# Performance work log

Hardware: AMD Instinct MI355X
Metric: run time of the kernel (lower is better)

The kernel has to match this reference:

```python
import jax, jax.numpy as jnp
import numpy as np

SEQ_LEN = 2048
EMB = 512
BATCH = 8


def _xavier_uniform(key, shape):
    fan_in, fan_out = shape[0], shape[1]
    bound = float(np.sqrt(6.0 / (fan_in + fan_out)))
    return jax.random.uniform(key, shape, dtype=jnp.float32, minval=-bound, maxval=bound)


def setup_inputs() -> dict:
    key = jax.random.key(0)
    kx, k1, k2 = jax.random.split(key, 3)
    x = jax.random.normal(kx, (BATCH, EMB, SEQ_LEN), dtype=jnp.float32)
    weight1 = _xavier_uniform(k1, (EMB, EMB))
    weight2 = _xavier_uniform(k2, (EMB, EMB))
    return {"x": x, "weight1": weight1, "weight2": weight2}


def reference(x, weight1, weight2):
    # x: [b, e, s]
    s = x.shape[-1]
    # projections: O(b*s*e^2)
    fitnesses1 = jnp.einsum('bes,ef->bfs', x, weight1)   # [b, e, s]
    fitnesses2 = jnp.einsum('bfs,ef->bes', x, weight2)   # [b, e, s]
    # s x t interaction matrix: O(b*s^2*e)
    weight = jnp.einsum('bes,bet->bst', fitnesses1, fitnesses2)  # [b, s, t]
    # zero strictly-upper triangle (t > s), as in torch.triu(..., diagonal=1)
    mask = jnp.triu(jnp.ones((s, s), dtype=bool), k=1)
    weight = jnp.where(mask, jnp.zeros((), dtype=weight.dtype), weight)
    fitnesses = jnp.einsum('bst,bet->bes', weight, x)    # [b, e, s]
    avg_fitness = jnp.einsum('bes,bes->be', x, fitnesses)[..., None]  # [b, e, 1]
    net_fitnesses = fitnesses - avg_fitness
    x_next = x + x * net_fitnesses
    return jax.nn.relu(x_next)
```

## Files before the change

### kernel.cpp

```cpp
#include <hip/hip_runtime.h>
#include <hip/hip_bf16.h>
#include <stdint.h>


#define SEQ 2048
#define EMB 512
#define NBATCH 8

typedef unsigned short u16;
typedef __bf16 bf16x8 __attribute__((ext_vector_type(8)));
typedef float f32x4 __attribute__((ext_vector_type(4)));
typedef u16 u16x8 __attribute__((ext_vector_type(8)));

#define AS1 __attribute__((address_space(1)))
#define AS3 __attribute__((address_space(3)))

#define SBAR do { __builtin_amdgcn_sched_barrier(0); __builtin_amdgcn_s_barrier(); \
                  __builtin_amdgcn_sched_barrier(0); } while (0)
#define LGKM0 do { asm volatile("s_waitcnt lgkmcnt(0)" ::: "memory"); \
                   __builtin_amdgcn_sched_barrier(0); } while (0)

__device__ __forceinline__ u16 f2bf(float f) {
  uint32_t u = __builtin_bit_cast(uint32_t, f);
  uint32_t r = u + 0x7FFFu + ((u >> 16) & 1u);
  return (u16)(r >> 16);
}
__device__ __forceinline__ float bf2f(u16 u) {
  return __builtin_bit_cast(float, (uint32_t)u << 16);
}
__device__ __forceinline__ void gld_lds16(const void* g, void* l) {
  __builtin_amdgcn_global_load_lds((AS1 uint32_t*)g, (AS3 uint32_t*)l, 16, 0, 0);
}

__global__ __launch_bounds__(256) void prep_x_kernel(const float* __restrict__ x,
    u16* __restrict__ xb, u16* __restrict__ xbT) {
  __shared__ float tile[64][65];
  const int b = blockIdx.z;
  const int s0 = blockIdx.x * 64, e0 = blockIdx.y * 64;
  const float* xin = x + (size_t)b * EMB * SEQ;
  const int tid = threadIdx.x;
  #pragma unroll
  for (int it = 0; it < 4; ++it) {
    int idx = it * 256 + tid;
    int r = idx >> 4, c4 = idx & 15;
    float4 v = *(const float4*)(xin + (size_t)(e0 + r) * SEQ + s0 + c4 * 4);
    tile[r][c4 * 4 + 0] = v.x; tile[r][c4 * 4 + 1] = v.y;
    tile[r][c4 * 4 + 2] = v.z; tile[r][c4 * 4 + 3] = v.w;
  }
  __syncthreads();
  u16* ob = xb + (size_t)b * EMB * SEQ;
  #pragma unroll
  for (int it = 0; it < 2; ++it) {
    int idx = it * 256 + tid; int r = idx >> 3, c8 = idx & 7;
    u16x8 o;
    #pragma unroll
    for (int q = 0; q < 8; ++q) o[q] = f2bf(tile[r][c8 * 8 + q]);
    *(u16x8*)(ob + (size_t)(e0 + r) * SEQ + s0 + c8 * 8) = o;
  }
  u16* obT = xbT + (size_t)b * SEQ * EMB;
  #pragma unroll
  for (int it = 0; it < 2; ++it) {
    int idx = it * 256 + tid; int r = idx >> 3, c8 = idx & 7;
    u16x8 o;
    #pragma unroll
    for (int q = 0; q < 8; ++q) o[q] = f2bf(tile[c8 * 8 + q][r]);
    *(u16x8*)(obT + (size_t)(s0 + r) * EMB + e0 + c8 * 8) = o;
  }
}

__global__ __launch_bounds__(256) void prep_w_kernel(const float* __restrict__ W1,
    const float* __restrict__ W2, u16* __restrict__ Wcat) {
  __shared__ float tile[32][33];
  const int c0 = blockIdx.x * 32, r0 = blockIdx.y * 32;
  const int tx = threadIdx.x, ty = threadIdx.y;
  if (blockIdx.z == 0) {
    #pragma unroll
    for (int i = 0; i < 32; i += 8)
      tile[ty + i][tx] = W1[(size_t)(r0 + ty + i) * EMB + c0 + tx];
    __syncthreads();
    #pragma unroll
    for (int i = 0; i < 32; i += 8)
      Wcat[(size_t)(c0 + ty + i) * EMB + r0 + tx] = f2bf(tile[tx][ty + i]);
  } else {
    u16* W2b = Wcat + (size_t)512 * 512;
    #pragma unroll
    for (int i = 0; i < 32; i += 8)
      W2b[(size_t)(r0 + ty + i) * EMB + c0 + tx] =
          f2bf(W2[(size_t)(r0 + ty + i) * EMB + c0 + tx]);
  }
}

struct Smem {
  __align__(16) u16 LA[2][256 * 64];
  __align__(16) u16 LB[2][256 * 64];
};

template<typename PAR>
__device__ __forceinline__ void gemm_pipe(PAR par, int nk, Smem& sm, f32x4 (&acc)[8][4]) {
  const int tid  = threadIdx.x;
  const int lane = tid & 63;
  const int wave = tid >> 6;
  const int wr = wave >> 2;
  const int wc = wave & 3;

  auto stage_half = [&](int t, int ab, int half, u16* lds) {
    const u16* g; int ld, k;
    par(t, ab, g, ld, k);
    #pragma unroll
    for (int p = 0; p < 2; ++p) {
      int c = p * 512 + tid;
      int row = c >> 3, cc = c & 7;
      int cs = cc ^ (row & 7);
      gld_lds16(g + (size_t)(half * 128 + row) * ld + k + cs * 8,
                lds + (size_t)(p * 512 + wave * 64) * 8);
    }
  };
  auto ldfrag = [&](const u16* base, int rloc, int c2) -> bf16x8 {
    int cs = c2 ^ (rloc & 7);
    return *reinterpret_cast<const bf16x8*>(base + (size_t)(rloc * 8 + cs) * 8);
  };

  stage_half(0, 0, 0, sm.LA[0]);
  stage_half(0, 0, 1, sm.LA[0] + 8192);
  stage_half(0, 1, 0, sm.LB[0]);
  stage_half(0, 1, 1, sm.LB[0] + 8192);
  if (nk > 1) {
    stage_half(1, 1, 0, sm.LB[1]);
    stage_half(1, 1, 1, sm.LB[1] + 8192);
  }
  if (nk > 1) { asm volatile("s_waitcnt vmcnt(4)" ::: "memory"); }
  else        { asm volatile("s_waitcnt vmcnt(0)" ::: "memory"); }
  SBAR;

  const int ar = lane & 15;
  const int asel = lane >> 4;
  bf16x8 af[4][2], bf0[2][2], bf1[2][2];

  for (int t = 0; t < nk; ++t) {
    const int sel = t & 1;
    const u16* a_ = sm.LA[sel];
    const u16* b_ = sm.LB[sel];

    #pragma unroll
    for (int m = 0; m < 4; ++m)
      #pragma unroll
      for (int kk = 0; kk < 2; ++kk)
        af[m][kk] = ldfrag(a_, wr * 128 + m * 16 + ar, kk * 4 + asel);
    #pragma unroll
    for (int n = 0; n < 2; ++n)
      #pragma unroll
      for (int kk = 0; kk < 2; ++kk)
        bf0[n][kk] = ldfrag(b_, wc * 64 + n * 16 + ar, kk * 4 + asel);
    if (t + 1 < nk) stage_half(t + 1, 0, 0, sm.LA[sel ^ 1]);
    SBAR; LGKM0;
    __builtin_amdgcn_s_setprio(1);
    #pragma unroll
    for (int m = 0; m < 4; ++m)
      #pragma unroll
      for (int n = 0; n < 2; ++n)
        #pragma unroll
        for (int kk = 0; kk < 2; ++kk)
          acc[m][n] = __builtin_amdgcn_mfma_f32_16x16x32_bf16(af[m][kk], bf0[n][kk], acc[m][n], 0, 0, 0);
    __builtin_amdgcn_s_setprio(0);
    SBAR;

    #pragma unroll
    for (int n = 0; n < 2; ++n)
      #pragma unroll
      for (int kk = 0; kk < 2; ++kk)
        bf1[n][kk] = ldfrag(b_, wc * 64 + (n + 2) * 16 + ar, kk * 4 + asel);
    if (t + 1 < nk) stage_half(t + 1, 0, 1, sm.LA[sel ^ 1] + 8192);
    SBAR; LGKM0;
    __builtin_amdgcn_s_setprio(1);
    #pragma unroll
    for (int m = 0; m < 4; ++m)
      #pragma unroll
      for (int n = 0; n < 2; ++n)
        #pragma unroll
        for (int kk = 0; kk < 2; ++kk)
          acc[m][n + 2] = __builtin_amdgcn_mfma_f32_16x16x32_bf16(af[m][kk], bf1[n][kk], acc[m][n + 2], 0, 0, 0);
    __builtin_amdgcn_s_setprio(0);
    SBAR;

    #pragma unroll
    for (int m = 0; m < 4; ++m)
      #pragma unroll
      for (int kk = 0; kk < 2; ++kk)
        af[m][kk] = ldfrag(a_, wr * 128 + 64 + m * 16 + ar, kk * 4 + asel);
    if (t + 2 < nk) stage_half(t + 2, 1, 0, sm.LB[sel]);
    SBAR; LGKM0;
    __builtin_amdgcn_s_setprio(1);
    #pragma unroll
    for (int m = 0; m < 4; ++m)
      #pragma unroll
      for (int n = 0; n < 2; ++n)
        #pragma unroll
        for (int kk = 0; kk < 2; ++kk)
          acc[m + 4][n + 2] = __builtin_amdgcn_mfma_f32_16x16x32_bf16(af[m][kk], bf1[n][kk], acc[m + 4][n + 2], 0, 0, 0);
    __builtin_amdgcn_s_setprio(0);
    SBAR;

    if (t + 2 < nk) stage_half(t + 2, 1, 1, sm.LB[sel] + 8192);
    SBAR;
    __builtin_amdgcn_s_setprio(1);
    #pragma unroll
    for (int m = 0; m < 4; ++m)
      #pragma unroll
      for (int n = 0; n < 2; ++n)
        #pragma unroll
        for (int kk = 0; kk < 2; ++kk)
          acc[m + 4][n] = __builtin_amdgcn_mfma_f32_16x16x32_bf16(af[m][kk], bf0[n][kk], acc[m + 4][n], 0, 0, 0);
    __builtin_amdgcn_s_setprio(0);
    if (t + 1 < nk) {
      if (t + 2 < nk) { asm volatile("s_waitcnt vmcnt(4)" ::: "memory"); }
      else            { asm volatile("s_waitcnt vmcnt(0)" ::: "memory"); }
    }
    SBAR;
  }
}

template<int MODE>
__global__ __launch_bounds__(512, 2) void k_gemm(
    const u16* __restrict__ X1, const u16* __restrict__ X2,
    const u16* __restrict__ X3, const u16* __restrict__ X4,
    u16* __restrict__ O16, u16* __restrict__ O16b) {
  __shared__ Smem sm;
  const int tid  = threadIdx.x;
  const int lane = tid & 63;
  const int wave = tid >> 6;
  const int wr = wave >> 2;
  const int wc = wave & 3;
  const int bz = blockIdx.z;

  f32x4 acc[8][4];
  #pragma unroll
  for (int i = 0; i < 8; ++i)
    #pragma unroll
    for (int j = 0; j < 4; ++j) acc[i][j] = (f32x4){0.f, 0.f, 0.f, 0.f};

  const int r0 = (lane >> 4) * 4;
  const int cn = lane & 15;

  if (MODE == 0) {
    const int xx = blockIdx.x;
    const u16* Ap; const u16* Bp;
    if (xx < 32) {
      const int m = xx >> 2, n = xx & 3;
      Ap = X1 + (size_t)bz * SEQ * EMB + (size_t)(m * 256) * 512;
      Bp = X2 + (size_t)(n * 256) * 512;
      auto par = [&](int t, int ab, const u16*& g, int& ld, int& k) {
        g = ab ? Bp : Ap; ld = 512; k = t * 64;
      };
      gemm_pipe(par, 8, sm, acc);
      u16* C = O16 + (size_t)bz * SEQ * 1024;
      #pragma unroll
      for (int mm = 0; mm < 8; ++mm)
        #pragma unroll
        for (int nn = 0; nn < 4; ++nn)
          #pragma unroll
          for (int r = 0; r < 4; ++r) {
            int lr = wr * 128 + mm * 16 + r0 + r, lc = wc * 64 + nn * 16 + cn;
            C[(size_t)(m * 256 + lr) * 1024 + n * 256 + lc] = f2bf(acc[mm][nn][r]);
          }
    } else {
      const int m2 = (xx - 32) >> 3, n2 = (xx - 32) & 7;
      Ap = X2 + (size_t)512 * 512 + (size_t)(m2 * 256) * 512;
      Bp = X1 + (size_t)bz * SEQ * EMB + (size_t)(n2 * 256) * 512;
      auto par = [&](int t, int ab, const u16*& g, int& ld, int& k) {
        g = ab ? Bp : Ap; ld = 512; k = t * 64;
      };
      gemm_pipe(par, 8, sm, acc);
      u16* C = O16b + (size_t)bz * EMB * SEQ;
      #pragma unroll
      for (int mm = 0; mm < 8; ++mm)
        #pragma unroll
        for (int nn = 0; nn < 4; ++nn)
          #pragma unroll
          for (int r = 0; r < 4; ++r) {
            int lr = wr * 128 + mm * 16 + r0 + r, lc = wc * 64 + nn * 16 + cn;
            C[(size_t)(m2 * 256 + lr) * SEQ + n2 * 256 + lc] = f2bf(acc[mm][nn][r]);
          }
    }
  } else if (MODE == 1) {
    const int xx = blockIdx.x;
    if (xx < 8) {
      const int i = xx;
      const u16* Fb = X1 + (size_t)bz * SEQ * 1024;
      const u16* Ap = Fb + (size_t)(i * 256) * 1024;
      const u16* Bp = Fb + 512 + (size_t)(i * 256) * 1024;
      auto par = [&](int t, int ab, const u16*& g, int& ld, int& k) {
        g = ab ? Bp : Ap; ld = 1024; k = t * 64;
      };
      gemm_pipe(par, 8, sm, acc);
      u16* C = O16 + (size_t)(bz * 8 + i) * 256 * 256;
      #pragma unroll
      for (int mm = 0; mm < 8; ++mm)
        #pragma unroll
        for (int nn = 0; nn < 4; ++nn)
          #pragma unroll
          for (int r = 0; r < 4; ++r) {
            int lr = wr * 128 + mm * 16 + r0 + r, lc = wc * 64 + nn * 16 + cn;
            float v = (lc > lr) ? 0.f : acc[mm][nn][r];
            C[(size_t)lr * 256 + lc] = f2bf(v);
          }
    } else {
      const int y = xx - 8;
      const int j = y >> 2, m = (y >> 1) & 1, n = y & 1;
      const u16* Ap = X2 + (size_t)bz * EMB * SEQ + (size_t)(m * 256) * SEQ + j * 256;
      const u16* Bp = X3 + (size_t)bz * EMB * SEQ + (size_t)(n * 256) * SEQ + j * 256;
      auto par = [&](int t, int ab, const u16*& g, int& ld, int& k) {
        g = ab ? Bp : Ap; ld = SEQ; k = t * 64;
      };
      gemm_pipe(par, 4, sm, acc);
      u16* C = O16b + (size_t)(bz * 8 + j) * EMB * EMB;
      #pragma unroll
      for (int mm = 0; mm < 8; ++mm)
        #pragma unroll
        for (int nn = 0; nn < 4; ++nn)
          #pragma unroll
          for (int r = 0; r < 4; ++r) {
            int lr = wr * 128 + mm * 16 + r0 + r, lc = wc * 64 + nn * 16 + cn;
            C[(size_t)(m * 256 + lr) * EMB + n * 256 + lc] = f2bf(acc[mm][nn][r]);
          }
    }
  } else {
    const int i = blockIdx.x >> 1, m = blockIdx.x & 1;
    const u16* Agp = (i > 0) ? X1 + (size_t)(bz * 7 + i - 1) * EMB * EMB + (size_t)(m * 256) * 512
                             : X1;
    const u16* Bf1 = X2 + (size_t)bz * SEQ * 1024 + (size_t)(i * 256) * 1024;
    const u16* Axb = X3 + (size_t)bz * EMB * SEQ + (size_t)(m * 256) * SEQ;
    const u16* Bsd = X4 + (size_t)(bz * 8 + i) * 256 * 256;
    auto par = [&](int t, int ab, const u16*& g, int& ld, int& k) {
      int tt = (i > 0) ? t : t + 8;
      if (tt < 8) {
        if (!ab) { g = Agp; ld = 512;  k = tt * 64; }
        else     { g = Bf1; ld = 1024; k = tt * 64; }
      } else {
        int u = tt - 8;
        if (!ab) { g = Axb; ld = SEQ; k = i * 256 + u * 64; }
        else     { g = Bsd; ld = 256; k = u * 64; }
      }
    };
    gemm_pipe(par, (i > 0) ? 12 : 4, sm, acc);
    u16* C = O16 + (size_t)bz * EMB * SEQ;
    #pragma unroll
    for (int mm = 0; mm < 8; ++mm)
      #pragma unroll
      for (int nn = 0; nn < 4; ++nn)
        #pragma unroll
        for (int r = 0; r < 4; ++r) {
          int lr = wr * 128 + mm * 16 + r0 + r, lc = wc * 64 + nn * 16 + cn;
          C[(size_t)(m * 256 + lr) * SEQ + i * 256 + lc] = f2bf(acc[mm][nn][r]);
        }
  }
}

__global__ __launch_bounds__(256) void k_prefix(const u16* __restrict__ Gc,
                                                u16* __restrict__ Gp) {
  const int b = blockIdx.z;
  const size_t base = ((size_t)blockIdx.x * 256 + threadIdx.x) * 8;
  float run[8] = {0.f, 0.f, 0.f, 0.f, 0.f, 0.f, 0.f, 0.f};
  #pragma unroll
  for (int j = 0; j < 7; ++j) {
    u16x8 v = *(const u16x8*)(Gc + (size_t)(b * 8 + j) * EMB * EMB + base);
    u16x8 o;
    #pragma unroll
    for (int q = 0; q < 8; ++q) { run[q] += bf2f(v[q]); o[q] = f2bf(run[q]); }
    *(u16x8*)(Gp + (size_t)(b * 7 + j) * EMB * EMB + base) = o;
  }
}

__global__ __launch_bounds__(256) void finalize_kernel(const u16* __restrict__ xb,
    const u16* __restrict__ fitb, float* __restrict__ out) {
  const size_t row = blockIdx.x;
  const u16* xr = xb + row * SEQ;
  const u16* fr = fitb + row * SEQ;
  float* orow = out + row * SEQ;
  const int tid = threadIdx.x;

  float xv[2][4], fv[2][4];
  float part = 0.f;
  #pragma unroll
  for (int i = 0; i < 2; ++i) {
    const int s0 = i * 1024 + tid * 4;
    ushort4 xu = *reinterpret_cast<const ushort4*>(xr + s0);
    ushort4 fu = *reinterpret_cast<const ushort4*>(fr + s0);
    xv[i][0] = bf2f(xu.x); xv[i][1] = bf2f(xu.y); xv[i][2] = bf2f(xu.z); xv[i][3] = bf2f(xu.w);
    fv[i][0] = bf2f(fu.x); fv[i][1] = bf2f(fu.y); fv[i][2] = bf2f(fu.z); fv[i][3] = bf2f(fu.w);
    part += xv[i][0] * fv[i][0] + xv[i][1] * fv[i][1] + xv[i][2] * fv[i][2] + xv[i][3] * fv[i][3];
  }
  #pragma unroll
  for (int off = 1; off < 64; off <<= 1) part += __shfl_xor(part, off);
  __shared__ float wsum[4];
  const int wave = tid >> 6, lane = tid & 63;
  if (lane == 0) wsum[wave] = part;
  __syncthreads();
  const float avg = wsum[0] + wsum[1] + wsum[2] + wsum[3];

  #pragma unroll
  for (int i = 0; i < 2; ++i) {
    float4 o;
    o.x = xv[i][0] * (1.f + fv[i][0] - avg); o.x = o.x > 0.f ? o.x : 0.f;
    o.y = xv[i][1] * (1.f + fv[i][1] - avg); o.y = o.y > 0.f ? o.y : 0.f;
    o.z = xv[i][2] * (1.f + fv[i][2] - avg); o.z = o.z > 0.f ? o.z : 0.f;
    o.w = xv[i][3] * (1.f + fv[i][3] - avg); o.w = o.w > 0.f ? o.w : 0.f;
    reinterpret_cast<float4*>(orow)[i * 256 + tid] = o;
  }
}

extern "C" void kernel_launch(void* const* d_in, const int* in_sizes, int n_in,
                              void* d_out, int out_size, void* d_ws, size_t ws_size,
                              hipStream_t stream) {
  const float* x  = (const float*)d_in[0];
  const float* W1 = (const float*)d_in[1];
  const float* W2 = (const float*)d_in[2];
  float* out = (float*)d_out;

  char* ws = (char*)d_ws;
  const size_t nX = (size_t)NBATCH * EMB * SEQ;

  size_t off = 0;
  u16* xb   = (u16*)(ws + off); off += nX * 2;
  u16* Fcat = (u16*)(ws + off); off += (size_t)NBATCH * SEQ * 1024 * 2;
  const size_t offOverlay = off;
  u16* xbT  = (u16*)(ws + off); off += nX * 2;
  u16* Wcat = (u16*)(ws + off); off += (size_t)1024 * 512 * 2;
  u16* F2n  = (u16*)(ws + off); off += nX * 2;
  u16* Sd   = (u16*)(ws + off); off += (size_t)NBATCH * 8 * 256 * 256 * 2;
  u16* Gc   = (u16*)(ws + off); off += (size_t)NBATCH * 8 * EMB * EMB * 2;
  u16* Gp   = (u16*)(ws + off); off += (size_t)NBATCH * 7 * EMB * EMB * 2;
  u16* fitb = (u16*)(ws + offOverlay);

  prep_x_kernel<<<dim3(SEQ / 64, EMB / 64, NBATCH), 256, 0, stream>>>(x, xb, xbT);
  prep_w_kernel<<<dim3(16, 16, 2), dim3(32, 8), 0, stream>>>(W1, W2, Wcat);

  k_gemm<0><<<dim3(48, 1, NBATCH), 512, 0, stream>>>(
      xbT, Wcat, nullptr, nullptr, Fcat, F2n);

  k_gemm<1><<<dim3(40, 1, NBATCH), 512, 0, stream>>>(
      Fcat, xb, F2n, nullptr, Sd, Gc);

  k_prefix<<<dim3(128, 1, NBATCH), 256, 0, stream>>>(Gc, Gp);

  k_gemm<2><<<dim3(16, 1, NBATCH), 512, 0, stream>>>(
      Gp, Fcat, xb, Sd, fitb, nullptr);

  finalize_kernel<<<NBATCH * EMB, 256, 0, stream>>>(xb, fitb, out);
}
```

Before: 135.4 us.

## Switch GEMM pipeline to 4-stage ring with K=32 tiles and single barrier

Replaces the double-buffered K=64 GEMM pipeline, which had four barrier-separated sub-phases per step, with a 4-deep LDS ring of K=32 tiles. Each step now issues one load and one MFMA phase with a single barrier, and prefetches three stages ahead. A new swizzle packs two rows per 128-byte line. Block index decoding is also reorganised into (x, g) groups so that each launch's grid mapping changes. The intent is to cut barrier overhead and hide global latency better, at the cost of twice as many K iterations and smaller per-step MFMA batches.

```diff
diff --git a/kernel.cpp b/kernel.cpp
--- a/kernel.cpp
+++ b/kernel.cpp
@@ -91,129 +91,62 @@
 }
 
 struct Smem {
-  __align__(16) u16 LA[2][256 * 64];
-  __align__(16) u16 LB[2][256 * 64];
+  __align__(16) u16 A[4][8192];
+  __align__(16) u16 B[4][8192];
 };
 
 template<typename PAR>
 __device__ __forceinline__ void gemm_pipe(PAR par, int nk, Smem& sm, f32x4 (&acc)[8][4]) {
-  const int tid  = threadIdx.x;
-  const int lane = tid & 63;
-  const int wave = tid >> 6;
-  const int wr = wave >> 2;
-  const int wc = wave & 3;
-
-  auto stage_half = [&](int t, int ab, int half, u16* lds) {
-    const u16* g; int ld, k;
-    par(t, ab, g, ld, k);
+  const int tid = threadIdx.x, lane = tid & 63, wave = tid >> 6;
+  const int wr = wave >> 2, wc = wave & 3;
+  const int ar = lane & 15, asel = lane >> 4;
+
+  auto stage = [&](int t) {
+    const u16 *ga, *gb; int lda, ldb, ka, kb;
+    par(t, 0, ga, lda, ka);
+    par(t, 1, gb, ldb, kb);
+    u16* LA = sm.A[t & 3];
+    u16* LB = sm.B[t & 3];
     #pragma unroll
     for (int p = 0; p < 2; ++p) {
-      int c = p * 512 + tid;
-      int row = c >> 3, cc = c & 7;
-      int cs = cc ^ (row & 7);
-      gld_lds16(g + (size_t)(half * 128 + row) * ld + k + cs * 8,
-                lds + (size_t)(p * 512 + wave * 64) * 8);
+      int idx = p * 512 + tid;
+      int line = idx >> 3, cp = (idx & 7) ^ (line & 7);
+      int row = line * 2 + (cp >> 2), cc = cp & 3;
+      gld_lds16(ga + (size_t)row * lda + ka + cc * 8, LA + (size_t)(p * 512 + wave * 64) * 8);
+      gld_lds16(gb + (size_t)row * ldb + kb + cc * 8, LB + (size_t)(p * 512 + wave * 64) * 8);
     }
   };
-  auto ldfrag = [&](const u16* base, int rloc, int c2) -> bf16x8 {
-    int cs = c2 ^ (rloc & 7);
-    return *reinterpret_cast<const bf16x8*>(base + (size_t)(rloc * 8 + cs) * 8);
+  auto ldfrag = [&](const u16* base, int rloc) -> bf16x8 {
+    int line = rloc >> 1;
+    int ch = line * 8 + ((((rloc & 1) << 2) | asel) ^ (line & 7));
+    return *reinterpret_cast<const bf16x8*>(base + (size_t)ch * 8);
   };
 
-  stage_half(0, 0, 0, sm.LA[0]);
-  stage_half(0, 0, 1, sm.LA[0] + 8192);
-  stage_half(0, 1, 0, sm.LB[0]);
-  stage_half(0, 1, 1, sm.LB[0] + 8192);
-  if (nk > 1) {
-    stage_half(1, 1, 0, sm.LB[1]);
-    stage_half(1, 1, 1, sm.LB[1] + 8192);
-  }
-  if (nk > 1) { asm volatile("s_waitcnt vmcnt(4)" ::: "memory"); }
-  else        { asm volatile("s_waitcnt vmcnt(0)" ::: "memory"); }
+  stage(0); stage(1); stage(2);
+  asm volatile("s_waitcnt vmcnt(8)" ::: "memory");
   SBAR;
 
-  const int ar = lane & 15;
-  const int asel = lane >> 4;
-  bf16x8 af[4][2], bf0[2][2], bf1[2][2];
-
   for (int t = 0; t < nk; ++t) {
-    const int sel = t & 1;
-    const u16* a_ = sm.LA[sel];
-    const u16* b_ = sm.LB[sel];
-
-    #pragma unroll
-    for (int m = 0; m < 4; ++m)
-      #pragma unroll
-      for (int kk = 0; kk < 2; ++kk)
-        af[m][kk] = ldfrag(a_, wr * 128 + m * 16 + ar, kk * 4 + asel);
-    #pragma unroll
-    for (int n = 0; n < 2; ++n)
-      #pragma unroll
-      for (int kk = 0; kk < 2; ++kk)
-        bf0[n][kk] = ldfrag(b_, wc * 64 + n * 16 + ar, kk * 4 + asel);
-    if (t + 1 < nk) stage_half(t + 1, 0, 0, sm.LA[sel ^ 1]);
-    SBAR; LGKM0;
+    const u16* A = sm.A[t & 3];
+    const u16* B = sm.B[t & 3];
+    bf16x8 af[8], bf[4];
+    #pragma unroll
+    for (int m = 0; m < 8; ++m) af[m] = ldfrag(A, wr * 128 + m * 16 + ar);
+    #pragma unroll
+    for (int n = 0; n < 4; ++n) bf[n] = ldfrag(B, wc * 64 + n * 16 + ar);
+    if (t + 3 < nk) stage(t + 3);
+    LGKM0;
     __builtin_amdgcn_s_setprio(1);
     #pragma unroll
-    for (int m = 0; m < 4; ++m)
-      #pragma unroll
-      for (int n = 0; n < 2; ++n)
-        #pragma unroll
-        for (int kk = 0; kk < 2; ++kk)
-          acc[m][n] = __builtin_amdgcn_mfma_f32_16x16x32_bf16(af[m][kk], bf0[n][kk], acc[m][n], 0, 0, 0);
-    __builtin_amdgcn_s_setprio(0);
-    SBAR;
-
-    #pragma unroll
-    for (int n = 0; n < 2; ++n)
-      #pragma unroll
-      for (int kk = 0; kk < 2; ++kk)
-        bf1[n][kk] = ldfrag(b_, wc * 64 + (n + 2) * 16 + ar, kk * 4 + asel);
-    if (t + 1 < nk) stage_half(t + 1, 0, 1, sm.LA[sel ^ 1] + 8192);
-    SBAR; LGKM0;
-    __builtin_amdgcn_s_setprio(1);
-    #pragma unroll
-    for (int m = 0; m < 4; ++m)
-      #pragma unroll
-      for (int n = 0; n < 2; ++n)
-        #pragma unroll
-        for (int kk = 0; kk < 2; ++kk)
-          acc[m][n + 2] = __builtin_amdgcn_mfma_f32_16x16x32_bf16(af[m][kk], bf1[n][kk], acc[m][n + 2], 0, 0, 0);
-    __builtin_amdgcn_s_setprio(0);
-    SBAR;
-
-    #pragma unroll
-    for (int m = 0; m < 4; ++m)
-      #pragma unroll
-      for (int kk = 0; kk < 2; ++kk)
-        af[m][kk] = ldfrag(a_, wr * 128 + 64 + m * 16 + ar, kk * 4 + asel);
-    if (t + 2 < nk) stage_half(t + 2, 1, 0, sm.LB[sel]);
-    SBAR; LGKM0;
-    __builtin_amdgcn_s_setprio(1);
-    #pragma unroll
-    for (int m = 0; m < 4; ++m)
-      #pragma unroll
-      for (int n = 0; n < 2; ++n)
-        #pragma unroll
-        for (int kk = 0; kk < 2; ++kk)
-          acc[m + 4][n + 2] = __builtin_amdgcn_mfma_f32_16x16x32_bf16(af[m][kk], bf1[n][kk], acc[m + 4][n + 2], 0, 0, 0);
-    __builtin_amdgcn_s_setprio(0);
-    SBAR;
-
-    if (t + 2 < nk) stage_half(t + 2, 1, 1, sm.LB[sel] + 8192);
-    SBAR;
-    __builtin_amdgcn_s_setprio(1);
-    #pragma unroll
-    for (int m = 0; m < 4; ++m)
-      #pragma unroll
-      for (int n = 0; n < 2; ++n)
-        #pragma unroll
-        for (int kk = 0; kk < 2; ++kk)
-          acc[m + 4][n] = __builtin_amdgcn_mfma_f32_16x16x32_bf16(af[m][kk], bf0[n][kk], acc[m + 4][n], 0, 0, 0);
+    for (int m = 0; m < 8; ++m)
+      #pragma unroll
+      for (int n = 0; n < 4; ++n)
+        acc[m][n] = __builtin_amdgcn_mfma_f32_16x16x32_bf16(af[m], bf[n], acc[m][n], 0, 0, 0);
     __builtin_amdgcn_s_setprio(0);
     if (t + 1 < nk) {
-      if (t + 2 < nk) { asm volatile("s_waitcnt vmcnt(4)" ::: "memory"); }
-      else            { asm volatile("s_waitcnt vmcnt(0)" ::: "memory"); }
+      if (t + 3 < nk)      { asm volatile("s_waitcnt vmcnt(8)" ::: "memory"); }
+      else if (t + 2 < nk) { asm volatile("s_waitcnt vmcnt(4)" ::: "memory"); }
+      else                 { asm volatile("s_waitcnt vmcnt(0)" ::: "memory"); }
     }
     SBAR;
   }
@@ -231,6 +164,7 @@
   const int wr = wave >> 2;
   const int wc = wave & 3;
   const int bz = blockIdx.z;
+  const int x = blockIdx.x & 7, g = blockIdx.x >> 3;
 
   f32x4 acc[8][4];
   #pragma unroll
@@ -242,16 +176,19 @@
   const int cn = lane & 15;
 
   if (MODE == 0) {
-    const int xx = blockIdx.x;
-    const u16* Ap; const u16* Bp;
-    if (xx < 32) {
-      const int m = xx >> 2, n = xx & 3;
-      Ap = X1 + (size_t)bz * SEQ * EMB + (size_t)(m * 256) * 512;
-      Bp = X2 + (size_t)(n * 256) * 512;
-      auto par = [&](int t, int ab, const u16*& g, int& ld, int& k) {
-        g = ab ? Bp : Ap; ld = 512; k = t * 64;
-      };
-      gemm_pipe(par, 8, sm, acc);
+    const u16 *Ap, *Bp;
+    if (g < 4) {
+      Ap = X1 + (size_t)bz * SEQ * EMB + (size_t)(x * 256) * 512;
+      Bp = X2 + (size_t)(g * 256) * 512;
+    } else {
+      Ap = X2 + (size_t)512 * 512 + (size_t)((g - 4) * 256) * 512;
+      Bp = X1 + (size_t)bz * SEQ * EMB + (size_t)(x * 256) * 512;
+    }
+    auto par = [&](int t, int ab, const u16*& gp, int& ld, int& k) {
+      gp = ab ? Bp : Ap; ld = 512; k = t * 32;
+    };
+    gemm_pipe(par, 16, sm, acc);
+    if (g < 4) {
       u16* C = O16 + (size_t)bz * SEQ * 1024;
       #pragma unroll
       for (int mm = 0; mm < 8; ++mm)
@@ -260,16 +197,9 @@
           #pragma unroll
           for (int r = 0; r < 4; ++r) {
             int lr = wr * 128 + mm * 16 + r0 + r, lc = wc * 64 + nn * 16 + cn;
-            C[(size_t)(m * 256 + lr) * 1024 + n * 256 + lc] = f2bf(acc[mm][nn][r]);
+            C[(size_t)(x * 256 + lr) * 1024 + g * 256 + lc] = f2bf(acc[mm][nn][r]);
           }
     } else {
-      const int m2 = (xx - 32) >> 3, n2 = (xx - 32) & 7;
-      Ap = X2 + (size_t)512 * 512 + (size_t)(m2 * 256) * 512;
-      Bp = X1 + (size_t)bz * SEQ * EMB + (size_t)(n2 * 256) * 512;
-      auto par = [&](int t, int ab, const u16*& g, int& ld, int& k) {
-        g = ab ? Bp : Ap; ld = 512; k = t * 64;
-      };
-      gemm_pipe(par, 8, sm, acc);
       u16* C = O16b + (size_t)bz * EMB * SEQ;
       #pragma unroll
       for (int mm = 0; mm < 8; ++mm)
@@ -278,21 +208,19 @@
           #pragma unroll
           for (int r = 0; r < 4; ++r) {
             int lr = wr * 128 + mm * 16 + r0 + r, lc = wc * 64 + nn * 16 + cn;
-            C[(size_t)(m2 * 256 + lr) * SEQ + n2 * 256 + lc] = f2bf(acc[mm][nn][r]);
+            C[(size_t)((g - 4) * 256 + lr) * SEQ + x * 256 + lc] = f2bf(acc[mm][nn][r]);
           }
     }
   } else if (MODE == 1) {
-    const int xx = blockIdx.x;
-    if (xx < 8) {
-      const int i = xx;
+    if (g == 0) {
       const u16* Fb = X1 + (size_t)bz * SEQ * 1024;
-      const u16* Ap = Fb + (size_t)(i * 256) * 1024;
-      const u16* Bp = Fb + 512 + (size_t)(i * 256) * 1024;
-      auto par = [&](int t, int ab, const u16*& g, int& ld, int& k) {
-        g = ab ? Bp : Ap; ld = 1024; k = t * 64;
+      const u16* Ap = Fb + (size_t)(x * 256) * 1024;
+      const u16* Bp = Fb + 512 + (size_t)(x * 256) * 1024;
+      auto par = [&](int t, int ab, const u16*& gp, int& ld, int& k) {
+        gp = ab ? Bp : Ap; ld = 1024; k = t * 32;
       };
-      gemm_pipe(par, 8, sm, acc);
-      u16* C = O16 + (size_t)(bz * 8 + i) * 256 * 256;
+      gemm_pipe(par, 16, sm, acc);
+      u16* C = O16 + (size_t)(bz * 8 + x) * 256 * 256;
       #pragma unroll
       for (int mm = 0; mm < 8; ++mm)
         #pragma unroll
@@ -304,15 +232,14 @@
             C[(size_t)lr * 256 + lc] = f2bf(v);
           }
     } else {
-      const int y = xx - 8;
-      const int j = y >> 2, m = (y >> 1) & 1, n = y & 1;
-      const u16* Ap = X2 + (size_t)bz * EMB * SEQ + (size_t)(m * 256) * SEQ + j * 256;
-      const u16* Bp = X3 + (size_t)bz * EMB * SEQ + (size_t)(n * 256) * SEQ + j * 256;
-      auto par = [&](int t, int ab, const u16*& g, int& ld, int& k) {
-        g = ab ? Bp : Ap; ld = SEQ; k = t * 64;
+      const int m = (g - 1) >> 1, n = (g - 1) & 1;
+      const u16* Ap = X2 + (size_t)bz * EMB * SEQ + (size_t)(m * 256) * SEQ + x * 256;
+      const u16* Bp = X3 + (size_t)bz * EMB * SEQ + (size_t)(n * 256) * SEQ + x * 256;
+      auto par = [&](int t, int ab, const u16*& gp, int& ld, int& k) {
+        gp = ab ? Bp : Ap; ld = SEQ; k = t * 32;
       };
-      gemm_pipe(par, 4, sm, acc);
-      u16* C = O16b + (size_t)(bz * 8 + j) * EMB * EMB;
+      gemm_pipe(par, 8, sm, acc);
+      u16* C = O16b + (size_t)(bz * 8 + x) * EMB * EMB;
       #pragma unroll
       for (int mm = 0; mm < 8; ++mm)
         #pragma unroll
@@ -324,24 +251,24 @@
           }
     }
   } else {
-    const int i = blockIdx.x >> 1, m = blockIdx.x & 1;
+    const int i = x, m = g;
     const u16* Agp = (i > 0) ? X1 + (size_t)(bz * 7 + i - 1) * EMB * EMB + (size_t)(m * 256) * 512
                              : X1;
     const u16* Bf1 = X2 + (size_t)bz * SEQ * 1024 + (size_t)(i * 256) * 1024;
     const u16* Axb = X3 + (size_t)bz * EMB * SEQ + (size_t)(m * 256) * SEQ;
     const u16* Bsd = X4 + (size_t)(bz * 8 + i) * 256 * 256;
-    auto par = [&](int t, int ab, const u16*& g, int& ld, int& k) {
-      int tt = (i > 0) ? t : t + 8;
-      if (tt < 8) {
-        if (!ab) { g = Agp; ld = 512;  k = tt * 64; }
-        else     { g = Bf1; ld = 1024; k = tt * 64; }
+    auto par = [&](int t, int ab, const u16*& gp, int& ld, int& k) {
+      int tt = (i > 0) ? t : t + 16;
+      if (tt < 16) {
+        if (!ab) { gp = Agp; ld = 512;  k = tt * 32; }
+        else     { gp = Bf1; ld = 1024; k = tt * 32; }
       } else {
-        int u = tt - 8;
-        if (!ab) { g = Axb; ld = SEQ; k = i * 256 + u * 64; }
-        else     { g = Bsd; ld = 256; k = u * 64; }
+        int u = tt - 16;
+        if (!ab) { gp = Axb; ld = SEQ; k = i * 256 + u * 32; }
+        else     { gp = Bsd; ld = 256; k = u * 32; }
       }
     };
-    gemm_pipe(par, (i > 0) ? 12 : 4, sm, acc);
+    gemm_pipe(par, (i > 0) ? 24 : 8, sm, acc);
     u16* C = O16 + (size_t)bz * EMB * SEQ;
     #pragma unroll
     for (int mm = 0; mm < 8; ++mm)
```

New measurement: 133.4 us. About the same (-1.5%).
